# Kernel tuning notes

Measured on AMD Instinct MI355X. Metric: run time of the kernel, lower is better.

## Reference

```python
import jax, jax.numpy as jnp
import numpy as np


def gcn_conv(x, edge_index, W, b):
    # PyG GCNConv with normalize=True: add self-loops, symmetric D^-1/2 A D^-1/2,
    # transform then aggregate messages source->target, then add bias.
    N = x.shape[0]
    row, col = edge_index[0], edge_index[1]  # row: source, col: target
    loop = jnp.arange(N, dtype=edge_index.dtype)
    row = jnp.concatenate([row, loop])
    col = jnp.concatenate([col, loop])
    ones = jnp.ones(row.shape[0], dtype=x.dtype)
    deg = jax.ops.segment_sum(ones, col, num_segments=N)
    dinv = jnp.where(deg > 0, jax.lax.rsqrt(deg), 0.0)
    norm = dinv[row] * dinv[col]            # [E+N]
    h = x @ W                                # [N, d_out] transform first (cheaper aggregation)
    msgs = h[row] * norm[:, None]            # gather + scale
    out = jax.ops.segment_sum(msgs, col, num_segments=N)  # scatter-add to targets
    return out + b


def setup_inputs() -> dict:
    key = jax.random.key(0)
    k = jax.random.split(key, 6)
    N, D, H, C, E = 100000, 256, 32, 2, 3200000
    x = jax.random.normal(k[0], (N, D), dtype=jnp.float32)
    edge_index = jax.random.randint(k[1], (2, E), 0, N, dtype=jnp.int64)
    # glorot-style init for GCN weights
    W1 = jax.random.normal(k[2], (D, H), dtype=jnp.float32) * np.sqrt(2.0 / (D + H))
    b1 = jnp.zeros((H,), dtype=jnp.float32)
    W2 = jax.random.normal(k[3], (H, C), dtype=jnp.float32) * np.sqrt(2.0 / (H + C))
    b2 = jnp.zeros((C,), dtype=jnp.float32)
    return {"x": x, "edge_index": edge_index, "W1": W1, "b1": b1, "W2": W2, "b2": b2}


def reference(x, edge_index, W1, b1, W2, b2):
    # CRD: GCNConv -> relu -> dropout(p=0.5, eval mode -> identity)
    h = jax.nn.relu(gcn_conv(x, edge_index, W1, b1))
    # CLS: GCNConv -> log_softmax over classes
    logits = gcn_conv(h, edge_index, W2, b2)
    return jax.nn.log_softmax(logits, axis=1)
```

## Files before the change

### kernel.cpp

```cpp
#include <hip/hip_runtime.h>
#include <hip/hip_fp16.h>
#include <math.h>

#define DIV_UP(a,b) (((a)+(b)-1)/(b))

typedef _Float16 f16x8 __attribute__((ext_vector_type(8)));
typedef float    f32x4 __attribute__((ext_vector_type(4)));

#define SHIFT 9
#define TPB   (1 << SHIFT)
#define LMASK (TPB - 1)
#define CHUNK 4096

__global__ __launch_bounds__(256) void k_init(int* __restrict__ gcur, int cap,
                                              int* __restrict__ offsets, int N, int E) {
    const int t = threadIdx.x;
    gcur[t] = t * cap;
    if (t == 0) offsets[N] = E;
}

__global__ __launch_bounds__(256) void k_fat(const float* __restrict__ x,
                                             const float* __restrict__ W,
                                             __half* __restrict__ h1,
                                             const int* __restrict__ row,
                                             const int* __restrict__ col,
                                             int* __restrict__ gcur,
                                             unsigned* __restrict__ binned,
                                             int E, int N, int nchunk) {
    __shared__ __align__(16) char smem[24608];
    const int t = threadIdx.x;
    const int bid = blockIdx.x;
    const bool isBin = (bid < 2 * nchunk) && (bid & 1);

    if (!isBin) {
        const int gb = (bid < 2 * nchunk) ? (bid >> 1) : (bid - nchunk);
        _Float16* WlT = (_Float16*)smem;

#pragma unroll
        for (int i = 0; i < 8; ++i) {
            int idx = t + 256 * i;
            float4 v = ((const float4*)W)[idx];
            int k  = idx >> 3;
            int n4 = (idx & 7) * 4;
            int kc = k >> 5, q = (k >> 3) & 3, j = k & 7;
            int ct = n4 >> 4, m0 = n4 & 15;
            _Float16* dst = WlT + ((size_t)((kc * 2 + ct) * 64 + q * 16 + m0) * 8 + j);
            dst[0 * 8] = (_Float16)v.x;
            dst[1 * 8] = (_Float16)v.y;
            dst[2 * 8] = (_Float16)v.z;
            dst[3 * 8] = (_Float16)v.w;
        }
        __syncthreads();

        const int lane = t & 63;
        const int wv   = t >> 6;
        const int m    = lane & 15;
        const int q    = lane >> 4;

        const int rowA   = gb * 64 + wv * 16 + m;
        const int rclamp = min(rowA, N - 1);
        const float* xr  = x + (long long)rclamp * 256 + q * 8;

        f32x4 c0 = {0.f, 0.f, 0.f, 0.f}, c1 = {0.f, 0.f, 0.f, 0.f};
#pragma unroll
        for (int kc = 0; kc < 8; ++kc) {
            float4 v0 = *(const float4*)(xr + kc * 32);
            float4 v1 = *(const float4*)(xr + kc * 32 + 4);
            f16x8 b0 = *(const f16x8*)&WlT[(size_t)((kc * 2 + 0) * 64 + lane) * 8];
            f16x8 b1 = *(const f16x8*)&WlT[(size_t)((kc * 2 + 1) * 64 + lane) * 8];
            f16x8 a;
            a[0] = (_Float16)v0.x; a[1] = (_Float16)v0.y;
            a[2] = (_Float16)v0.z; a[3] = (_Float16)v0.w;
            a[4] = (_Float16)v1.x; a[5] = (_Float16)v1.y;
            a[6] = (_Float16)v1.z; a[7] = (_Float16)v1.w;
            c0 = __builtin_amdgcn_mfma_f32_16x16x32_f16(a, b0, c0, 0, 0, 0);
            c1 = __builtin_amdgcn_mfma_f32_16x16x32_f16(a, b1, c1, 0, 0, 0);
        }

        const int orow = gb * 64 + wv * 16 + q * 4;
#pragma unroll
        for (int r = 0; r < 4; ++r) {
            int gr = orow + r;
            if (gr < N) {
                h1[gr * 32 + m]      = __float2half(c0[r]);
                h1[gr * 32 + 16 + m] = __float2half(c1[r]);
            }
        }
    } else {
        int* hist  = (int*)smem;
        int* loff  = hist + 256;
        int* gbase = loff + 256;
        int* lcur  = gbase + 256;
        unsigned* staged     = (unsigned*)(smem + 4096);
        unsigned char* binOf = (unsigned char*)(smem + 4096 + 16384);
        int* wtot            = (int*)(smem + 4096 + 16384 + 4096);

        const int base = (bid >> 1) * CHUNK;
        const int n = min(CHUNK, E - base);

        hist[t] = 0;
        __syncthreads();

        unsigned pk[CHUNK / 256];
        int bn[CHUNK / 256];
#pragma unroll
        for (int k = 0; k < CHUNK / 256; ++k) {
            int i = base + t + k * 256;
            if (i < E) {
                int c = col[i], r = row[i];
                bn[k] = c >> SHIFT;
                pk[k] = ((unsigned)r << SHIFT) | (unsigned)(c & LMASK);
                atomicAdd(&hist[bn[k]], 1);
            } else bn[k] = -1;
        }
        __syncthreads();

        const int hv = hist[t];
        int sc = hv;
#pragma unroll
        for (int s = 1; s < 64; s <<= 1) {
            int y = __shfl_up(sc, s, 64);
            if ((t & 63) >= s) sc += y;
        }
        if ((t & 63) == 63) wtot[t >> 6] = sc;
        __syncthreads();
        int woff = 0;
#pragma unroll
        for (int j = 0; j < 3; ++j) if (j < (t >> 6)) woff += wtot[j];
        const int excl = sc + woff - hv;
        gbase[t] = hv ? atomicAdd(&gcur[t], hv) : 0;
        lcur[t] = excl;
        loff[t] = excl;
        __syncthreads();

#pragma unroll
        for (int k = 0; k < CHUNK / 256; ++k) {
            if (bn[k] >= 0) {
                int p = atomicAdd(&lcur[bn[k]], 1);
                staged[p] = pk[k];
                binOf[p] = (unsigned char)bn[k];
            }
        }
        __syncthreads();

        for (int i = t; i < n; i += 256) {
            int bb = binOf[i];
            binned[gbase[bb] + (i - loff[bb])] = staged[i];
        }
    }
}

__global__ __launch_bounds__(1024) void k_csr2(const unsigned* __restrict__ binned,
                                               const int* __restrict__ gcur, int cap,
                                               int* __restrict__ offsets,
                                               float* __restrict__ dinv,
                                               int* __restrict__ srcs,
                                               __half* __restrict__ h1, int N) {
    __shared__ int h[TPB];
    __shared__ int cur[TPB];
    __shared__ float sdi[TPB];
    __shared__ int wred[16];
    const int t = threadIdx.x, b = blockIdx.x;
    const int lane = t & 63, wv = t >> 6;
    const int beg = b * cap, end = gcur[b];

    int contrib = (t < 256 && t < b) ? (gcur[t] - t * cap) : 0;
#pragma unroll
    for (int s = 1; s < 64; s <<= 1) contrib += __shfl_xor(contrib, s, 64);
    if (t < TPB) h[t] = 0;
    if (lane == 0 && wv < 4) wred[wv] = contrib;
    __syncthreads();
    const int obase = wred[0] + wred[1] + wred[2] + wred[3];

    for (int i = beg + t; i < end; i += 1024)
        atomicAdd(&h[binned[i] & LMASK], 1);
    __syncthreads();

    const int cnt = (t < TPB) ? h[t] : 0;
    int sc = cnt;
#pragma unroll
    for (int s = 1; s < 64; s <<= 1) {
        int y = __shfl_up(sc, s, 64);
        if (lane >= s) sc += y;
    }
    if (t < TPB && lane == 63) wred[8 + wv] = sc;
    __syncthreads();
    if (t < TPB) {
        int woff = 0;
        for (int j = 0; j < wv; ++j) woff += wred[8 + j];
        const int excl = sc + woff - cnt;
        const int g = (b << SHIFT) + t;
        const int pos0 = obase + excl;
        float di = 0.f;
        if (g < N) {
            offsets[g] = pos0;
            di = rsqrtf((float)(1 + cnt));
            dinv[g] = di;
        }
        cur[t] = pos0;
        sdi[t] = di;
    }
    __syncthreads();

    for (int i = beg + t; i < end; i += 1024) {
        unsigned v = binned[i];
        int pos = atomicAdd(&cur[v & LMASK], 1);
        srcs[pos] = (int)(v >> SHIFT);
    }

    const int node = (b << SHIFT) + (t >> 1);
    if (node < N) {
        float di = sdi[t >> 1];
        uint4* hp4 = (uint4*)(h1 + (size_t)node * 32) + (t & 1) * 2;
#pragma unroll
        for (int k4 = 0; k4 < 2; ++k4) {
            uint4 v = hp4[k4];
            __half2* ph = (__half2*)&v;
#pragma unroll
            for (int k2 = 0; k2 < 4; ++k2) {
                float2 u = __half22float2(ph[k2]);
                ph[k2] = __floats2half2_rn(u.x * di, u.y * di);
            }
            hp4[k4] = v;
        }
    }
}

__global__ void k_agg1(const int* __restrict__ offsets, const int* __restrict__ srcs,
                       const float* __restrict__ dinv, const __half* __restrict__ h1w,
                       const float* __restrict__ b1, const float* __restrict__ W2,
                       __half2* __restrict__ tw, int N) {
    long long g = (long long)blockIdx.x * blockDim.x + threadIdx.x;
    int node = (int)(g >> 5), f = (int)(g & 31);
    if (node >= N) return;
    const int sub = f >> 2, q = f & 3;
    const int beg = offsets[node], end = offsets[node + 1];
    const uint4* h4 = (const uint4*)h1w;

    float a0 = 0.f, a1 = 0.f, a2 = 0.f, a3 = 0.f;
    float a4 = 0.f, a5 = 0.f, a6 = 0.f, a7 = 0.f;

    for (int j = beg; j < end; j += 16) {
        int e0 = j + sub, e1 = j + 8 + sub;
        int s0 = srcs[min(e0, end - 1)];
        int s1 = srcs[min(e1, end - 1)];
        float m0 = (e0 < end) ? 1.f : 0.f;
        float m1 = (e1 < end) ? 1.f : 0.f;
        uint4 rv0 = h4[s0 * 4 + q];
        uint4 rv1 = h4[s1 * 4 + q];
        __half2 p; float2 u;
        p = *(__half2*)&rv0.x; u = __half22float2(p); a0 = fmaf(u.x, m0, a0); a1 = fmaf(u.y, m0, a1);
        p = *(__half2*)&rv0.y; u = __half22float2(p); a2 = fmaf(u.x, m0, a2); a3 = fmaf(u.y, m0, a3);
        p = *(__half2*)&rv0.z; u = __half22float2(p); a4 = fmaf(u.x, m0, a4); a5 = fmaf(u.y, m0, a5);
        p = *(__half2*)&rv0.w; u = __half22float2(p); a6 = fmaf(u.x, m0, a6); a7 = fmaf(u.y, m0, a7);
        p = *(__half2*)&rv1.x; u = __half22float2(p); a0 = fmaf(u.x, m1, a0); a1 = fmaf(u.y, m1, a1);
        p = *(__half2*)&rv1.y; u = __half22float2(p); a2 = fmaf(u.x, m1, a2); a3 = fmaf(u.y, m1, a3);
        p = *(__half2*)&rv1.z; u = __half22float2(p); a4 = fmaf(u.x, m1, a4); a5 = fmaf(u.y, m1, a5);
        p = *(__half2*)&rv1.w; u = __half22float2(p); a6 = fmaf(u.x, m1, a6); a7 = fmaf(u.y, m1, a7);
    }
#pragma unroll
    for (int s = 4; s < 32; s <<= 1) {
        a0 += __shfl_xor(a0, s, 32); a1 += __shfl_xor(a1, s, 32);
        a2 += __shfl_xor(a2, s, 32); a3 += __shfl_xor(a3, s, 32);
        a4 += __shfl_xor(a4, s, 32); a5 += __shfl_xor(a5, s, 32);
        a6 += __shfl_xor(a6, s, 32); a7 += __shfl_xor(a7, s, 32);
    }
    if (sub == 0) {
        float di = dinv[node];
        uint4 rv = h4[node * 4 + q];
        float sf[8];
        {
            __half2 p; float2 u;
            p = *(__half2*)&rv.x; u = __half22float2(p); sf[0] = u.x; sf[1] = u.y;
            p = *(__half2*)&rv.y; u = __half22float2(p); sf[2] = u.x; sf[3] = u.y;
            p = *(__half2*)&rv.z; u = __half22float2(p); sf[4] = u.x; sf[5] = u.y;
            p = *(__half2*)&rv.w; u = __half22float2(p); sf[6] = u.x; sf[7] = u.y;
        }
        float av[8] = {a0, a1, a2, a3, a4, a5, a6, a7};
        float t0 = 0.f, t1 = 0.f;
#pragma unroll
        for (int k = 0; k < 8; ++k) {
            int feat = q * 8 + k;
            float hv = fmaf(di, av[k] + sf[k], b1[feat]);
            hv = fmaxf(hv, 0.f);
            t0 = fmaf(hv, W2[feat * 2 + 0], t0);
            t1 = fmaf(hv, W2[feat * 2 + 1], t1);
        }
        t0 += __shfl_xor(t0, 1, 32); t0 += __shfl_xor(t0, 2, 32);
        t1 += __shfl_xor(t1, 1, 32); t1 += __shfl_xor(t1, 2, 32);
        if (q == 0) tw[node] = __floats2half2_rn(di * t0, di * t1);
    }
}

__global__ __launch_bounds__(1024) void k_cls(const unsigned* __restrict__ binned,
                                              const int* __restrict__ gcur, int cap,
                                              const float* __restrict__ dinv,
                                              const __half2* __restrict__ tw,
                                              const float* __restrict__ b2,
                                              float* __restrict__ out, int N) {
    __shared__ float lacc[2 * TPB];
    const int t = threadIdx.x, b = blockIdx.x;
    lacc[t] = 0.f;
    __syncthreads();
    const int beg = b * cap, end = gcur[b];
    for (int i = beg + t; i < end; i += 1024) {
        unsigned v = binned[i];
        int loc = v & LMASK;
        float2 u = __half22float2(tw[v >> SHIFT]);
        atomicAdd(&lacc[2 * loc],     u.x);
        atomicAdd(&lacc[2 * loc + 1], u.y);
    }
    __syncthreads();
    if (t < TPB) {
        int g = (b << SHIFT) + t;
        if (g < N) {
            float di = dinv[g];
            float2 u = __half22float2(tw[g]);
            float z0 = di * (lacc[2 * t]     + u.x) + b2[0];
            float z1 = di * (lacc[2 * t + 1] + u.y) + b2[1];
            float m = fmaxf(z0, z1);
            float lse = m + logf(expf(z0 - m) + expf(z1 - m));
            ((float2*)out)[g] = float2{z0 - lse, z1 - lse};
        }
    }
}

extern "C" void kernel_launch(void* const* d_in, const int* in_sizes, int n_in,
                              void* d_out, int out_size, void* d_ws, size_t ws_size,
                              hipStream_t stream) {
    const float* x  = (const float*)d_in[0];
    const int*   ei = (const int*)d_in[1];
    const float* W1 = (const float*)d_in[2];
    const float* b1 = (const float*)d_in[3];
    const float* W2 = (const float*)d_in[4];
    const float* b2 = (const float*)d_in[5];

    const int H = in_sizes[3];
    const int D = in_sizes[2] / H;
    const int N = in_sizes[0] / D;
    const int E = in_sizes[1] / 2;
    (void)H; (void)n_in; (void)out_size; (void)ws_size;

    const int* row = ei;
    const int* col = ei + E;

    const int K_used = ((N - 1) >> SHIFT) + 1;
    const int cap    = (DIV_UP(E, K_used) * 5 / 4 + 255) & ~255;
    const int nchunk = DIV_UP(E, CHUNK);
    const int gemmB  = DIV_UP(N, 64);

    char* p = (char*)d_ws;
    auto alloc = [&](size_t bytes) { char* q = p; p += (bytes + 255) & ~(size_t)255; return q; };
    int*      offsets = (int*)     alloc((size_t)(N + 1) * 4);
    int*      gcur    = (int*)     alloc(256 * 4);
    float*    dinv    = (float*)   alloc((size_t)N * 4);
    unsigned* binned  = (unsigned*)alloc((size_t)K_used * cap * 4);
    __half*   h1      = (__half*)  alloc((size_t)N * 32 * 2);
    int*      srcs    = (int*)     alloc((size_t)E * 4);
    __half2*  tw      = (__half2*) alloc((size_t)N * 4);

    k_init <<<1, 256, 0, stream>>>(gcur, cap, offsets, N, E);
    k_fat  <<<gemmB + nchunk, 256, 0, stream>>>(x, W1, h1, row, col, gcur, binned, E, N, nchunk);
    k_csr2 <<<K_used, 1024, 0, stream>>>(binned, gcur, cap, offsets, dinv, srcs, h1, N);
    k_agg1 <<<(int)DIV_UP((long long)N * 32, 256), 256, 0, stream>>>(offsets, srcs, dinv, h1, b1, W2, tw, N);
    k_cls  <<<K_used, 1024, 0, stream>>>(binned, gcur, cap, dinv, tw, b2, (float*)d_out, N);
}
```

Measured before the change: 303.8 us.

## Replace CSR build and pull aggregation with binned shared-memory atomic scatter

Result: slower. 918.4 us (+202.3%).

```diff
diff --git a/kernel.cpp b/kernel.cpp
--- a/kernel.cpp
+++ b/kernel.cpp
@@ -12,11 +12,9 @@
 #define LMASK (TPB - 1)
 #define CHUNK 4096
 
-__global__ __launch_bounds__(256) void k_init(int* __restrict__ gcur, int cap,
-                                              int* __restrict__ offsets, int N, int E) {
+__global__ __launch_bounds__(256) void k_init(int* __restrict__ gcur, int cap) {
     const int t = threadIdx.x;
     gcur[t] = t * cap;
-    if (t == 0) offsets[N] = E;
 }
 
 __global__ __launch_bounds__(256) void k_fat(const float* __restrict__ x,
@@ -150,169 +148,137 @@
     }
 }
 
-__global__ __launch_bounds__(1024) void k_csr2(const unsigned* __restrict__ binned,
-                                               const int* __restrict__ gcur, int cap,
-                                               int* __restrict__ offsets,
-                                               float* __restrict__ dinv,
-                                               int* __restrict__ srcs,
-                                               __half* __restrict__ h1, int N) {
+__global__ __launch_bounds__(1024) void k_deg(const unsigned* __restrict__ binned,
+                                              const int* __restrict__ gcur, int cap,
+                                              float* __restrict__ dinv, int N) {
     __shared__ int h[TPB];
-    __shared__ int cur[TPB];
-    __shared__ float sdi[TPB];
-    __shared__ int wred[16];
-    const int t = threadIdx.x, b = blockIdx.x;
-    const int lane = t & 63, wv = t >> 6;
+    const int t = threadIdx.x, bb = blockIdx.x;
+    const int b = bb >> 1, half = bb & 1;
+    if (t < TPB) h[t] = 0;
+    __syncthreads();
     const int beg = b * cap, end = gcur[b];
-
-    int contrib = (t < 256 && t < b) ? (gcur[t] - t * cap) : 0;
-#pragma unroll
-    for (int s = 1; s < 64; s <<= 1) contrib += __shfl_xor(contrib, s, 64);
-    if (t < TPB) h[t] = 0;
-    if (lane == 0 && wv < 4) wred[wv] = contrib;
-    __syncthreads();
-    const int obase = wred[0] + wred[1] + wred[2] + wred[3];
-
     for (int i = beg + t; i < end; i += 1024)
         atomicAdd(&h[binned[i] & LMASK], 1);
     __syncthreads();
-
-    const int cnt = (t < TPB) ? h[t] : 0;
-    int sc = cnt;
-#pragma unroll
-    for (int s = 1; s < 64; s <<= 1) {
-        int y = __shfl_up(sc, s, 64);
-        if (lane >= s) sc += y;
-    }
-    if (t < TPB && lane == 63) wred[8 + wv] = sc;
-    __syncthreads();
-    if (t < TPB) {
-        int woff = 0;
-        for (int j = 0; j < wv; ++j) woff += wred[8 + j];
-        const int excl = sc + woff - cnt;
-        const int g = (b << SHIFT) + t;
-        const int pos0 = obase + excl;
-        float di = 0.f;
-        if (g < N) {
-            offsets[g] = pos0;
-            di = rsqrtf((float)(1 + cnt));
-            dinv[g] = di;
-        }
-        cur[t] = pos0;
-        sdi[t] = di;
-    }
-    __syncthreads();
-
-    for (int i = beg + t; i < end; i += 1024) {
-        unsigned v = binned[i];
-        int pos = atomicAdd(&cur[v & LMASK], 1);
-        srcs[pos] = (int)(v >> SHIFT);
-    }
-
-    const int node = (b << SHIFT) + (t >> 1);
-    if (node < N) {
-        float di = sdi[t >> 1];
-        uint4* hp4 = (uint4*)(h1 + (size_t)node * 32) + (t & 1) * 2;
-#pragma unroll
-        for (int k4 = 0; k4 < 2; ++k4) {
-            uint4 v = hp4[k4];
-            __half2* ph = (__half2*)&v;
-#pragma unroll
-            for (int k2 = 0; k2 < 4; ++k2) {
-                float2 u = __half22float2(ph[k2]);
-                ph[k2] = __floats2half2_rn(u.x * di, u.y * di);
-            }
-            hp4[k4] = v;
-        }
-    }
-}
-
-__global__ void k_agg1(const int* __restrict__ offsets, const int* __restrict__ srcs,
-                       const float* __restrict__ dinv, const __half* __restrict__ h1w,
-                       const float* __restrict__ b1, const float* __restrict__ W2,
-                       __half2* __restrict__ tw, int N) {
-    long long g = (long long)blockIdx.x * blockDim.x + threadIdx.x;
-    int node = (int)(g >> 5), f = (int)(g & 31);
-    if (node >= N) return;
-    const int sub = f >> 2, q = f & 3;
-    const int beg = offsets[node], end = offsets[node + 1];
-    const uint4* h4 = (const uint4*)h1w;
-
-    float a0 = 0.f, a1 = 0.f, a2 = 0.f, a3 = 0.f;
-    float a4 = 0.f, a5 = 0.f, a6 = 0.f, a7 = 0.f;
-
-    for (int j = beg; j < end; j += 16) {
-        int e0 = j + sub, e1 = j + 8 + sub;
-        int s0 = srcs[min(e0, end - 1)];
-        int s1 = srcs[min(e1, end - 1)];
-        float m0 = (e0 < end) ? 1.f : 0.f;
-        float m1 = (e1 < end) ? 1.f : 0.f;
-        uint4 rv0 = h4[s0 * 4 + q];
-        uint4 rv1 = h4[s1 * 4 + q];
-        __half2 p; float2 u;
-        p = *(__half2*)&rv0.x; u = __half22float2(p); a0 = fmaf(u.x, m0, a0); a1 = fmaf(u.y, m0, a1);
-        p = *(__half2*)&rv0.y; u = __half22float2(p); a2 = fmaf(u.x, m0, a2); a3 = fmaf(u.y, m0, a3);
-        p = *(__half2*)&rv0.z; u = __half22float2(p); a4 = fmaf(u.x, m0, a4); a5 = fmaf(u.y, m0, a5);
-        p = *(__half2*)&rv0.w; u = __half22float2(p); a6 = fmaf(u.x, m0, a6); a7 = fmaf(u.y, m0, a7);
-        p = *(__half2*)&rv1.x; u = __half22float2(p); a0 = fmaf(u.x, m1, a0); a1 = fmaf(u.y, m1, a1);
-        p = *(__half2*)&rv1.y; u = __half22float2(p); a2 = fmaf(u.x, m1, a2); a3 = fmaf(u.y, m1, a3);
-        p = *(__half2*)&rv1.z; u = __half22float2(p); a4 = fmaf(u.x, m1, a4); a5 = fmaf(u.y, m1, a5);
-        p = *(__half2*)&rv1.w; u = __half22float2(p); a6 = fmaf(u.x, m1, a6); a7 = fmaf(u.y, m1, a7);
-    }
-#pragma unroll
-    for (int s = 4; s < 32; s <<= 1) {
-        a0 += __shfl_xor(a0, s, 32); a1 += __shfl_xor(a1, s, 32);
-        a2 += __shfl_xor(a2, s, 32); a3 += __shfl_xor(a3, s, 32);
-        a4 += __shfl_xor(a4, s, 32); a5 += __shfl_xor(a5, s, 32);
-        a6 += __shfl_xor(a6, s, 32); a7 += __shfl_xor(a7, s, 32);
-    }
-    if (sub == 0) {
-        float di = dinv[node];
-        uint4 rv = h4[node * 4 + q];
-        float sf[8];
-        {
-            __half2 p; float2 u;
-            p = *(__half2*)&rv.x; u = __half22float2(p); sf[0] = u.x; sf[1] = u.y;
-            p = *(__half2*)&rv.y; u = __half22float2(p); sf[2] = u.x; sf[3] = u.y;
-            p = *(__half2*)&rv.z; u = __half22float2(p); sf[4] = u.x; sf[5] = u.y;
-            p = *(__half2*)&rv.w; u = __half22float2(p); sf[6] = u.x; sf[7] = u.y;
-        }
-        float av[8] = {a0, a1, a2, a3, a4, a5, a6, a7};
-        float t0 = 0.f, t1 = 0.f;
-#pragma unroll
-        for (int k = 0; k < 8; ++k) {
-            int feat = q * 8 + k;
-            float hv = fmaf(di, av[k] + sf[k], b1[feat]);
-            hv = fmaxf(hv, 0.f);
-            t0 = fmaf(hv, W2[feat * 2 + 0], t0);
-            t1 = fmaf(hv, W2[feat * 2 + 1], t1);
-        }
-        t0 += __shfl_xor(t0, 1, 32); t0 += __shfl_xor(t0, 2, 32);
-        t1 += __shfl_xor(t1, 1, 32); t1 += __shfl_xor(t1, 2, 32);
-        if (q == 0) tw[node] = __floats2half2_rn(di * t0, di * t1);
-    }
-}
-
-__global__ __launch_bounds__(1024) void k_cls(const unsigned* __restrict__ binned,
-                                              const int* __restrict__ gcur, int cap,
-                                              const float* __restrict__ dinv,
-                                              const __half2* __restrict__ tw,
-                                              const float* __restrict__ b2,
-                                              float* __restrict__ out, int N) {
-    __shared__ float lacc[2 * TPB];
-    const int t = threadIdx.x, b = blockIdx.x;
-    lacc[t] = 0.f;
-    __syncthreads();
+    if (t < 256) {
+        int g = (b << SHIFT) + (half << 8) + t;
+        if (g < N) dinv[g] = rsqrtf((float)(1 + h[(half << 8) + t]));
+    }
+}
+
+__global__ __launch_bounds__(1024) void k_agg1s(const unsigned* __restrict__ binned,
+                                                const int* __restrict__ gcur, int cap,
+                                                const float* __restrict__ dinv,
+                                                const __half* __restrict__ h1,
+                                                const float* __restrict__ b1,
+                                                const float* __restrict__ W2,
+                                                __half2* __restrict__ tw, int N) {
+    __shared__ float sAcc[256 * 32];
+    __shared__ float sW2[64];
+    __shared__ float sb1[32];
+    const int t = threadIdx.x, bb = blockIdx.x;
+    const int b = bb >> 1, half = bb & 1;
+
+#pragma unroll
+    for (int i = t; i < 8192; i += 1024) sAcc[i] = 0.f;
+    if (t < 64) sW2[t] = W2[t];
+    else if (t >= 64 && t < 96) sb1[t - 64] = b1[t - 64];
+    __syncthreads();
+
     const int beg = b * cap, end = gcur[b];
     for (int i = beg + t; i < end; i += 1024) {
         unsigned v = binned[i];
         int loc = v & LMASK;
-        float2 u = __half22float2(tw[v >> SHIFT]);
-        atomicAdd(&lacc[2 * loc],     u.x);
-        atomicAdd(&lacc[2 * loc + 1], u.y);
-    }
-    __syncthreads();
-    if (t < TPB) {
-        int g = (b << SHIFT) + t;
+        if ((loc >> 8) == half) {
+            int src = (int)(v >> SHIFT);
+            float di = dinv[src];
+            const uint4* r4 = (const uint4*)(h1 + (size_t)src * 32);
+            uint4 q0 = r4[0], q1 = r4[1], q2 = r4[2], q3 = r4[3];
+            int l8 = loc & 255;
+            float* ab = sAcc + l8 * 32;
+            float2 u;
+#define ACC8(Q, F0)                                                                           \
+            u = __half22float2(*(__half2*)&Q.x);                                              \
+            atomicAdd(&ab[((F0 + 0) + l8) & 31], di * u.x);                                   \
+            atomicAdd(&ab[((F0 + 1) + l8) & 31], di * u.y);                                   \
+            u = __half22float2(*(__half2*)&Q.y);                                              \
+            atomicAdd(&ab[((F0 + 2) + l8) & 31], di * u.x);                                   \
+            atomicAdd(&ab[((F0 + 3) + l8) & 31], di * u.y);                                   \
+            u = __half22float2(*(__half2*)&Q.z);                                              \
+            atomicAdd(&ab[((F0 + 4) + l8) & 31], di * u.x);                                   \
+            atomicAdd(&ab[((F0 + 5) + l8) & 31], di * u.y);                                   \
+            u = __half22float2(*(__half2*)&Q.w);                                              \
+            atomicAdd(&ab[((F0 + 6) + l8) & 31], di * u.x);                                   \
+            atomicAdd(&ab[((F0 + 7) + l8) & 31], di * u.y);
+            ACC8(q0, 0)
+            ACC8(q1, 8)
+            ACC8(q2, 16)
+            ACC8(q3, 24)
+#undef ACC8
+        }
+    }
+    __syncthreads();
+
+    if (t < 256) {
+        int g = (b << SHIFT) + (half << 8) + t;
+        if (g < N) {
+            float dig = dinv[g];
+            const uint4* r4 = (const uint4*)(h1 + (size_t)g * 32);
+            uint4 q0 = r4[0], q1 = r4[1], q2 = r4[2], q3 = r4[3];
+            const float* ar = sAcc + t * 32;
+            float t0 = 0.f, t1 = 0.f;
+            float2 u;
+#define FIN2(H2, K)                                                                           \
+            u = __half22float2(H2);                                                           \
+            {                                                                                 \
+                float a0 = ar[((K) + t) & 31];                                                \
+                float a1 = ar[((K) + 1 + t) & 31];                                            \
+                float h0 = fmaxf(fmaf(dig, a0 + dig * u.x, sb1[(K)]), 0.f);                   \
+                float h1v = fmaxf(fmaf(dig, a1 + dig * u.y, sb1[(K) + 1]), 0.f);              \
+                t0 = fmaf(h0, sW2[2 * (K)], t0);                                              \
+                t1 = fmaf(h0, sW2[2 * (K) + 1], t1);                                          \
+                t0 = fmaf(h1v, sW2[2 * ((K) + 1)], t0);                                       \
+                t1 = fmaf(h1v, sW2[2 * ((K) + 1) + 1], t1);                                   \
+            }
+            FIN2(*(__half2*)&q0.x, 0)  FIN2(*(__half2*)&q0.y, 2)
+            FIN2(*(__half2*)&q0.z, 4)  FIN2(*(__half2*)&q0.w, 6)
+            FIN2(*(__half2*)&q1.x, 8)  FIN2(*(__half2*)&q1.y, 10)
+            FIN2(*(__half2*)&q1.z, 12) FIN2(*(__half2*)&q1.w, 14)
+            FIN2(*(__half2*)&q2.x, 16) FIN2(*(__half2*)&q2.y, 18)
+            FIN2(*(__half2*)&q2.z, 20) FIN2(*(__half2*)&q2.w, 22)
+            FIN2(*(__half2*)&q3.x, 24) FIN2(*(__half2*)&q3.y, 26)
+            FIN2(*(__half2*)&q3.z, 28) FIN2(*(__half2*)&q3.w, 30)
+#undef FIN2
+            tw[g] = __floats2half2_rn(dig * t0, dig * t1);
+        }
+    }
+}
+
+__global__ __launch_bounds__(1024) void k_agg2s(const unsigned* __restrict__ binned,
+                                                const int* __restrict__ gcur, int cap,
+                                                const float* __restrict__ dinv,
+                                                const __half2* __restrict__ tw,
+                                                const float* __restrict__ b2,
+                                                float* __restrict__ out, int N) {
+    __shared__ float lacc[512];
+    const int t = threadIdx.x, bb = blockIdx.x;
+    const int b = bb >> 1, half = bb & 1;
+    if (t < 512) lacc[t] = 0.f;
+    __syncthreads();
+    const int beg = b * cap, end = gcur[b];
+    for (int i = beg + t; i < end; i += 1024) {
+        unsigned v = binned[i];
+        int loc = v & LMASK;
+        if ((loc >> 8) == half) {
+            float2 u = __half22float2(tw[v >> SHIFT]);
+            int l8 = loc & 255;
+            atomicAdd(&lacc[2 * l8],     u.x);
+            atomicAdd(&lacc[2 * l8 + 1], u.y);
+        }
+    }
+    __syncthreads();
+    if (t < 256) {
+        int g = (b << SHIFT) + (half << 8) + t;
         if (g < N) {
             float di = dinv[g];
             float2 u = __half22float2(tw[g]);
@@ -351,17 +317,15 @@
 
     char* p = (char*)d_ws;
     auto alloc = [&](size_t bytes) { char* q = p; p += (bytes + 255) & ~(size_t)255; return q; };
-    int*      offsets = (int*)     alloc((size_t)(N + 1) * 4);
     int*      gcur    = (int*)     alloc(256 * 4);
     float*    dinv    = (float*)   alloc((size_t)N * 4);
     unsigned* binned  = (unsigned*)alloc((size_t)K_used * cap * 4);
     __half*   h1      = (__half*)  alloc((size_t)N * 32 * 2);
-    int*      srcs    = (int*)     alloc((size_t)E * 4);
     __half2*  tw      = (__half2*) alloc((size_t)N * 4);
 
-    k_init <<<1, 256, 0, stream>>>(gcur, cap, offsets, N, E);
-    k_fat  <<<gemmB + nchunk, 256, 0, stream>>>(x, W1, h1, row, col, gcur, binned, E, N, nchunk);
-    k_csr2 <<<K_used, 1024, 0, stream>>>(binned, gcur, cap, offsets, dinv, srcs, h1, N);
-    k_agg1 <<<(int)DIV_UP((long long)N * 32, 256), 256, 0, stream>>>(offsets, srcs, dinv, h1, b1, W2, tw, N);
-    k_cls  <<<K_used, 1024, 0, stream>>>(binned, gcur, cap, dinv, tw, b2, (float*)d_out, N);
-}
+    k_init  <<<1, 256, 0, stream>>>(gcur, cap);
+    k_fat   <<<gemmB + nchunk, 256, 0, stream>>>(x, W1, h1, row, col, gcur, binned, E, N, nchunk);
+    k_deg   <<<2 * K_used, 1024, 0, stream>>>(binned, gcur, cap, dinv, N);
+    k_agg1s <<<2 * K_used, 1024, 0, stream>>>(binned, gcur, cap, dinv, h1, b1, W2, tw, N);
+    k_agg2s <<<2 * K_used, 1024, 0, stream>>>(binned, gcur, cap, dinv, tw, b2, (float*)d_out, N);
+}
```
